# Performance work log

Measured on AMD Instinct MI355X. Metric: run time of the kernel, lower is better.

## Reference

```python
import jax, jax.numpy as jnp
import numpy as np

NUM_HEADS = 16
ROPE_BASE = 10000.0


def _rope_cos_sin(seq_len, head_dim, dtype):
    # Rotary (cramming-style): inv_freq over even indices, emb = cat(freqs, freqs)
    inv_freq = 1.0 / (ROPE_BASE ** (jnp.arange(0, head_dim, 2, dtype=jnp.float32) / head_dim))
    t = jnp.arange(seq_len, dtype=jnp.float32)
    freqs = jnp.einsum('i,j->ij', t, inv_freq)          # [S, d/2]
    emb = jnp.concatenate([freqs, freqs], axis=-1)      # [S, d]
    # broadcast over batch and heads: [1, S, 1, d]
    return jnp.cos(emb)[None, :, None, :].astype(dtype), jnp.sin(emb)[None, :, None, :].astype(dtype)


def _rotate_half(x):
    d = x.shape[-1] // 2
    return jnp.concatenate([-x[..., d:], x[..., :d]], axis=-1)


def setup_inputs() -> dict:
    key = jax.random.key(0)
    k1, k2, k3 = jax.random.split(key, 3)
    B, S, D = 4, 1024, 1024
    hidden_states = jax.random.normal(k1, (B, S, D), dtype=jnp.float32)
    Wqkv = jax.random.normal(k2, (3 * D, D), dtype=jnp.float32) * (D ** -0.5)
    bqkv = jax.random.normal(k3, (3 * D,), dtype=jnp.float32) * 0.02
    return {"hidden_states": hidden_states, "Wqkv": Wqkv, "bqkv": bqkv}


def reference(hidden_states, Wqkv, bqkv):
    B, S, D = hidden_states.shape
    H = NUM_HEADS
    hd = D // H

    # QKV projection (nn.Linear: x @ W.T + b)
    qkv = hidden_states @ Wqkv.T + bqkv                  # [B, S, 3D]
    qkv = qkv.reshape(B, S, 3, H, hd)
    q, k, v = qkv[:, :, 0], qkv[:, :, 1], qkv[:, :, 2]   # [B, S, H, hd]

    # Rotary embedding on q, k
    cos, sin = _rope_cos_sin(S, hd, q.dtype)
    q = q * cos + _rotate_half(q) * sin
    k = k * cos + _rotate_half(k) * sin

    # Causal scaled-dot-product attention (math of FlashAttention)
    scale = hd ** -0.5
    scores = jnp.einsum('bqhd,bkhd->bhqk', q, k) * scale  # [B, H, S, S]
    causal_mask = jnp.tril(jnp.ones((S, S), dtype=bool))
    scores = jnp.where(causal_mask, scores, jnp.finfo(scores.dtype).min)
    probs = jax.nn.softmax(scores, axis=-1)
    context = jnp.einsum('bhqk,bkhd->bqhd', probs, v)     # [B, S, H, hd]

    return context.reshape(B, S, D)
```

## Files before the change

kernel.cpp:

```cpp
#include <hip/hip_runtime.h>
#include <hip/hip_bf16.h>
#include <stdint.h>

typedef float f32x4 __attribute__((ext_vector_type(4)));
typedef __bf16 bf16x8 __attribute__((ext_vector_type(8)));

#define MFMA(a, b, c) __builtin_amdgcn_mfma_f32_16x16x32_bf16((a), (b), (c), 0, 0, 0)

__device__ __forceinline__ bf16x8 ld8(const void* p) { return *(const bf16x8*)p; }

__device__ __forceinline__ bf16x8 ld8f(const float* p) {
    float4 a = *(const float4*)p;
    float4 b = *(const float4*)(p + 4);
    bf16x8 r;
    r[0] = (__bf16)a.x; r[1] = (__bf16)a.y; r[2] = (__bf16)a.z; r[3] = (__bf16)a.w;
    r[4] = (__bf16)b.x; r[5] = (__bf16)b.y; r[6] = (__bf16)b.z; r[7] = (__bf16)b.w;
    return r;
}

__device__ __forceinline__ float fexp2(float x) {
    float r;
    asm("v_exp_f32 %0, %1" : "=v"(r) : "v"(x));
    return r;
}

__device__ __forceinline__ void gload16(const void* g, void* l) {
    __builtin_amdgcn_global_load_lds(
        (const __attribute__((address_space(1))) void*)g,
        (__attribute__((address_space(3))) void*)l, 16, 0, 0);
}

#define SW(row, cb) ((((row) * 128) + (cb)) ^ (((row) & 7) << 4))
#define SWV(row, cb) (((row) * 128) + ((cb) ^ (((((row) & 7) ^ (((row) >> 3) & 7))) << 4)))

#define SCALE2 0.18033688011112042f

__global__ void convert2_kernel(const float* __restrict__ X,
                                const float* __restrict__ W,
                                __bf16* __restrict__ out,
                                float2* __restrict__ rope) {
    const int bid = blockIdx.x;
    if (bid < 3584) {
        const size_t i = (size_t)(bid * 256 + threadIdx.x) * 8;
        const size_t NX = (size_t)4096 * 1024;
        if (i < NX) *(bf16x8*)(out + i) = ld8f(X + i);
        else        *(bf16x8*)(out + i) = ld8f(W + (i - NX));
    } else {
        const int idx = (bid - 3584) * 256 + threadIdx.x;
        const int t = idx >> 5, j = idx & 31;
        const float invf = __expf(-(float)j * 0.28782313662425575f);
        const float ang = (float)t * invf;
        float s, c;
        sincosf(ang, &s, &c);
        rope[idx] = make_float2(c, s);
    }
}

__global__ void rope_table_kernel(float2* __restrict__ rope) {
    const int idx = blockIdx.x * 256 + threadIdx.x;
    const int t = idx >> 5, j = idx & 31;
    const float invf = __expf(-(float)j * 0.28782313662425575f);
    const float ang = (float)t * invf;
    float s, c;
    sincosf(ang, &s, &c);
    rope[idx] = make_float2(c, s);
}

__global__ __launch_bounds__(256, 5) void qkv_rope_fast(
    const __bf16* __restrict__ Xb,
    const __bf16* __restrict__ Wb,
    const float* __restrict__ bias,
    const float2* __restrict__ rope,
    __bf16* __restrict__ QKV)
{
    __shared__ __align__(16) __bf16 Asm[128 * 64];
    __shared__ __align__(16) __bf16 Bsm[64 * 64];
    const int tid = threadIdx.x;
    const int w = tid >> 6, lane = tid & 63;
    const int fr = lane & 15, fq = lane >> 4;
    const int bn = blockIdx.x, bm = blockIdx.y;

    const int lrow = lane >> 3;
    const int scol = (((lane & 7) ^ lrow) & 7) * 8;
    const __bf16* ga = Xb + (size_t)(bm * 128 + w * 32 + lrow) * 1024 + scol;
    const __bf16* gb = Wb + (size_t)(bn * 64 + w * 16 + lrow) * 1024 + scol;
    __bf16* lA = &Asm[w * 2048];
    __bf16* lB = &Bsm[w * 1024];
    const uint8_t* Ab = (const uint8_t*)Asm;
    const uint8_t* Bb = (const uint8_t*)Bsm;

    const f32x4 fzero = {0.f, 0.f, 0.f, 0.f};
    f32x4 acc[2][4];
#pragma unroll
    for (int i = 0; i < 2; ++i)
#pragma unroll
        for (int j = 0; j < 4; ++j) acc[i][j] = fzero;

    for (int kt = 0; kt < 16; ++kt) {
        __syncthreads();
#pragma unroll
        for (int i = 0; i < 4; ++i)
            gload16(ga + (size_t)(i * 8) * 1024 + kt * 64, lA + i * 512);
#pragma unroll
        for (int i = 0; i < 2; ++i)
            gload16(gb + (size_t)(i * 8) * 1024 + kt * 64, lB + i * 512);
        __syncthreads();

#pragma unroll
        for (int kk = 0; kk < 2; ++kk) {
            bf16x8 af[2], bg[4];
#pragma unroll
            for (int mi = 0; mi < 2; ++mi)
                af[mi] = ld8(&Ab[SW(w * 32 + mi * 16 + fr, kk * 64 + fq * 16)]);
#pragma unroll
            for (int ni = 0; ni < 4; ++ni)
                bg[ni] = ld8(&Bb[SW(ni * 16 + fr, kk * 64 + fq * 16)]);
#pragma unroll
            for (int mi = 0; mi < 2; ++mi)
#pragma unroll
                for (int ni = 0; ni < 4; ++ni)
                    acc[mi][ni] = MFMA(af[mi], bg[ni], acc[mi][ni]);
        }
    }

    const int n0 = bn * 64;
    const int region = n0 >> 10;
    float bia[4];
#pragma unroll
    for (int ni = 0; ni < 4; ++ni) bia[ni] = bias[n0 + ni * 16 + fr];
#pragma unroll
    for (int mi = 0; mi < 2; ++mi) {
#pragma unroll
        for (int jr = 0; jr < 4; ++jr) {
            const int rg = bm * 128 + w * 32 + mi * 16 + fq * 4 + jr;
            const int spos = rg & 1023;
            float v0 = acc[mi][0][jr] + bia[0];
            float v1 = acc[mi][1][jr] + bia[1];
            float v2 = acc[mi][2][jr] + bia[2];
            float v3 = acc[mi][3][jr] + bia[3];
            if (region < 2) {
                const float2 cs0 = rope[spos * 32 + fr];
                const float2 cs1 = rope[spos * 32 + 16 + fr];
                const float t0 = v0, t1 = v1;
                v0 = t0 * cs0.x - v2 * cs0.y;
                v2 = v2 * cs0.x + t0 * cs0.y;
                v1 = t1 * cs1.x - v3 * cs1.y;
                v3 = v3 * cs1.x + t1 * cs1.y;
                if (region == 0) {
                    v0 *= SCALE2; v1 *= SCALE2; v2 *= SCALE2; v3 *= SCALE2;
                }
            }
            __bf16* op = QKV + (size_t)rg * 3072 + n0 + fr;
            op[0]  = (__bf16)v0;
            op[16] = (__bf16)v1;
            op[32] = (__bf16)v2;
            op[48] = (__bf16)v3;
        }
    }
}

__global__ __launch_bounds__(256, 2) void qkv_rope_slow(
    const float* __restrict__ X, const float* __restrict__ W,
    const float* __restrict__ bias, const float2* __restrict__ rope,
    __bf16* __restrict__ QKV)
{
    __shared__ __align__(16) __bf16 Asm[128 * 64];
    __shared__ __align__(16) __bf16 Bsm[128 * 64];
    const int tid = threadIdx.x;
    const int w = tid >> 6, lane = tid & 63;
    const int fr = lane & 15, fq = lane >> 4;
    const int wr = w >> 1, wn = w & 1;
    const int bn = blockIdx.x, bm = blockIdx.y;
    const int srow = w * 32 + (lane >> 3);
    const int scol = (lane & 7) * 8;
    const float* ga = X + (size_t)(bm * 128 + srow) * 1024 + scol;
    const float* gb = W + (size_t)(bn * 128 + srow) * 1024 + scol;
    const int ldst = w * 2048 + lane * 8;

    const f32x4 fzero = {0.f, 0.f, 0.f, 0.f};
    f32x4 acc[4][4];
#pragma unroll
    for (int i = 0; i < 4; ++i)
#pragma unroll
        for (int j = 0; j < 4; ++j) acc[i][j] = fzero;

    for (int kt = 0; kt < 16; ++kt) {
        bf16x8 av[4], bv[4];
#pragma unroll
        for (int i = 0; i < 4; ++i) {
            av[i] = ld8f(ga + (size_t)(i * 8) * 1024 + kt * 64);
            bv[i] = ld8f(gb + (size_t)(i * 8) * 1024 + kt * 64);
        }
        __syncthreads();
#pragma unroll
        for (int i = 0; i < 4; ++i) {
            *(bf16x8*)&Asm[ldst + i * 512] = av[i];
            *(bf16x8*)&Bsm[ldst + i * 512] = bv[i];
        }
        __syncthreads();
        bf16x8 af[4][2], bg[4][2];
#pragma unroll
        for (int mi = 0; mi < 4; ++mi)
#pragma unroll
            for (int kk = 0; kk < 2; ++kk)
                af[mi][kk] = ld8(&Asm[(wr * 64 + mi * 16 + fr) * 64 + kk * 32 + fq * 8]);
#pragma unroll
        for (int ni = 0; ni < 4; ++ni)
#pragma unroll
            for (int kk = 0; kk < 2; ++kk)
                bg[ni][kk] = ld8(&Bsm[(wn * 64 + ni * 16 + fr) * 64 + kk * 32 + fq * 8]);
#pragma unroll
        for (int kk = 0; kk < 2; ++kk)
#pragma unroll
            for (int mi = 0; mi < 4; ++mi)
#pragma unroll
                for (int ni = 0; ni < 4; ++ni)
                    acc[mi][ni] = MFMA(af[mi][kk], bg[ni][kk], acc[mi][ni]);
    }

    const int n0 = bn * 128 + wn * 64;
    const int region = n0 >> 10;
    float bia[4];
#pragma unroll
    for (int ni = 0; ni < 4; ++ni) bia[ni] = bias[n0 + ni * 16 + fr];
#pragma unroll
    for (int mi = 0; mi < 4; ++mi) {
#pragma unroll
        for (int jr = 0; jr < 4; ++jr) {
            const int rg = bm * 128 + wr * 64 + mi * 16 + fq * 4 + jr;
            const int spos = rg & 1023;
            float v0 = acc[mi][0][jr] + bia[0];
            float v1 = acc[mi][1][jr] + bia[1];
            float v2 = acc[mi][2][jr] + bia[2];
            float v3 = acc[mi][3][jr] + bia[3];
            if (region < 2) {
                const float2 cs0 = rope[spos * 32 + fr];
                const float2 cs1 = rope[spos * 32 + 16 + fr];
                const float t0 = v0, t1 = v1;
                v0 = t0 * cs0.x - v2 * cs0.y;
                v2 = v2 * cs0.x + t0 * cs0.y;
                v1 = t1 * cs1.x - v3 * cs1.y;
                v3 = v3 * cs1.x + t1 * cs1.y;
                if (region == 0) {
                    v0 *= SCALE2; v1 *= SCALE2; v2 *= SCALE2; v3 *= SCALE2;
                }
            }
            __bf16* op = QKV + (size_t)rg * 3072 + n0 + fr;
            op[0]  = (__bf16)v0;
            op[16] = (__bf16)v1;
            op[32] = (__bf16)v2;
            op[48] = (__bf16)v3;
        }
    }
}

__global__ __launch_bounds__(256, 2) void attn_kernel(
    const __bf16* __restrict__ QKV,
    float* __restrict__ Out)
{
    __shared__ __align__(16) uint8_t smem[49152];
    const int tid = threadIdx.x;
    const int w = tid >> 6, lane = tid & 63;
    const int fr = lane & 15, fq = lane >> 4;
    const int b = blockIdx.x >> 4, h = blockIdx.x & 15;
    const int jp = blockIdx.y;
    const int qtA = jp, qtB = 15 - jp;
    const int q0A = qtA * 64, q0B = qtB * 64;
    const __bf16* base = QKV + (size_t)b * 1024 * 3072 + h * 64;

    bf16x8 qfA[2], qfB[2];
#pragma unroll
    for (int kk = 0; kk < 2; ++kk) {
        qfA[kk] = ld8(base + (size_t)(q0A + w * 16 + fr) * 3072 + kk * 32 + fq * 8);
        qfB[kk] = ld8(base + (size_t)(q0B + w * 16 + fr) * 3072 + kk * 32 + fq * 8);
    }

    const f32x4 fzero = {0.f, 0.f, 0.f, 0.f};
    f32x4 oA[4], oB[4];
    float lA[4], lB[4];
#pragma unroll
    for (int jr = 0; jr < 4; ++jr) { lA[jr] = 0.f; lB[jr] = 0.f; }
#pragma unroll
    for (int fn = 0; fn < 4; ++fn) { oA[fn] = fzero; oB[fn] = fzero; }

    const int skey = tid >> 3;
    const int scol = (tid & 7) * 8;
    const int nkt = qtB + 1;
    const int pbA = 32768 + w * 4096;
    const int pbB = pbA + 2048;

    {
        const size_t g0 = (size_t)skey * 3072;
        const size_t g1 = (size_t)(32 + skey) * 3072;
        bf16x8 kxa = ld8(base + g0 + 1024 + scol);
        bf16x8 kxb = ld8(base + g1 + 1024 + scol);
        bf16x8 vxa = ld8(base + g0 + 2048 + scol);
        bf16x8 vxb = ld8(base + g1 + 2048 + scol);
        *(bf16x8*)&smem[SW(skey, scol * 2)] = kxa;
        *(bf16x8*)&smem[SW(32 + skey, scol * 2)] = kxb;
#pragma unroll
        for (int jj = 0; jj < 8; ++jj) {
            *(__bf16*)&smem[8192 + SWV(scol + jj, skey * 2)] = vxa[jj];
            *(__bf16*)&smem[8192 + SWV(scol + jj, (32 + skey) * 2)] = vxb[jj];
        }
    }
    __syncthreads();

#define MASKEXP_WRITE(SV, Q0, PB)                                              \
    do {                                                                       \
        if ((k0 + 63) > ((Q0) + w * 16)) {                                     \
            _Pragma("unroll") for (int ni = 0; ni < 4; ++ni)                   \
                _Pragma("unroll") for (int jr = 0; jr < 4; ++jr) {             \
                    const int rg = (Q0) + w * 16 + fq * 4 + jr;                \
                    const int kg = k0 + ni * 16 + fr;                          \
                    if (kg > rg) SV[ni][jr] = -1.0e30f;                        \
                }                                                              \
        }                                                                      \
        _Pragma("unroll") for (int jr = 0; jr < 4; ++jr) {                     \
            float ts = 0.f;                                                    \
            _Pragma("unroll") for (int ni = 0; ni < 4; ++ni) {                 \
                const float p = fexp2(SV[ni][jr]);                             \
                SV[ni][jr] = p;                                                \
                ts += p;                                                       \
            }                                                                  \
            (PB == pbA ? lA : lB)[jr] += ts;                                   \
        }                                                                      \
        _Pragma("unroll") for (int ni = 0; ni < 4; ++ni)                       \
            _Pragma("unroll") for (int jr = 0; jr < 4; ++jr)                   \
                *(__bf16*)&smem[(PB) + SW(fq * 4 + jr, (ni * 16 + fr) * 2)] =  \
                    (__bf16)SV[ni][jr];                                        \
    } while (0)

    for (int kt = 0; kt < nkt; ++kt) {
        const int k0 = kt * 64;
        const int cb = (kt & 1) << 14;
        const int nb = cb ^ 16384;
        const bool dual = (kt <= qtA);

        bf16x8 kxa, kxb, vxa, vxb;
        const bool pre = (kt + 1 < nkt);
        if (pre) {
            const size_t g0 = (size_t)(k0 + 64 + skey) * 3072;
            const size_t g1 = (size_t)(k0 + 96 + skey) * 3072;
            kxa = ld8(base + g0 + 1024 + scol);
            kxb = ld8(base + g1 + 1024 + scol);
            vxa = ld8(base + g0 + 2048 + scol);
            vxb = ld8(base + g1 + 2048 + scol);
        }

        f32x4 svA[4], svB[4];
#pragma unroll
        for (int ni = 0; ni < 4; ++ni) { svA[ni] = fzero; svB[ni] = fzero; }
#pragma unroll
        for (int kk = 0; kk < 2; ++kk) {
            bf16x8 kf[4];
#pragma unroll
            for (int ni = 0; ni < 4; ++ni)
                kf[ni] = ld8(&smem[cb + SW(ni * 16 + fr, (kk * 32 + fq * 8) * 2)]);
#pragma unroll
            for (int ni = 0; ni < 4; ++ni)
                svB[ni] = MFMA(qfB[kk], kf[ni], svB[ni]);
            if (dual) {
#pragma unroll
                for (int ni = 0; ni < 4; ++ni)
                    svA[ni] = MFMA(qfA[kk], kf[ni], svA[ni]);
            }
        }

        MASKEXP_WRITE(svB, q0B, pbB);
        if (dual) MASKEXP_WRITE(svA, q0A, pbA);

#pragma unroll
        for (int ks = 0; ks < 2; ++ks) {
            bf16x8 vf[4];
#pragma unroll
            for (int fn = 0; fn < 4; ++fn)
                vf[fn] = ld8(&smem[cb + 8192 + SWV(fn * 16 + fr, (ks * 32 + fq * 8) * 2)]);
            bf16x8 pfB = ld8(&smem[pbB + SW(fr, (ks * 32 + fq * 8) * 2)]);
#pragma unroll
            for (int fn = 0; fn < 4; ++fn)
                oB[fn] = MFMA(pfB, vf[fn], oB[fn]);
            if (dual) {
                bf16x8 pfA = ld8(&smem[pbA + SW(fr, (ks * 32 + fq * 8) * 2)]);
#pragma unroll
                for (int fn = 0; fn < 4; ++fn)
                    oA[fn] = MFMA(pfA, vf[fn], oA[fn]);
            }
        }

        if (pre) {
            *(bf16x8*)&smem[nb + SW(skey, scol * 2)] = kxa;
            *(bf16x8*)&smem[nb + SW(32 + skey, scol * 2)] = kxb;
#pragma unroll
            for (int jj = 0; jj < 8; ++jj) {
                *(__bf16*)&smem[nb + 8192 + SWV(scol + jj, skey * 2)] = vxa[jj];
                *(__bf16*)&smem[nb + 8192 + SWV(scol + jj, (32 + skey) * 2)] = vxb[jj];
            }
        }
        __syncthreads();
    }
#undef MASKEXP_WRITE

#pragma unroll
    for (int jr = 0; jr < 4; ++jr) {
        float la = lA[jr], lb = lB[jr];
#pragma unroll
        for (int off = 1; off < 16; off <<= 1) {
            la += __shfl_xor(la, off, 64);
            lb += __shfl_xor(lb, off, 64);
        }
        const float invA = 1.0f / fmaxf(la, 1.0e-20f);
        const float invB = 1.0f / fmaxf(lb, 1.0e-20f);
        const int rgA = q0A + w * 16 + fq * 4 + jr;
        const int rgB = q0B + w * 16 + fq * 4 + jr;
        float* opA = Out + (size_t)(b * 1024 + rgA) * 1024 + h * 64 + fr;
        float* opB = Out + (size_t)(b * 1024 + rgB) * 1024 + h * 64 + fr;
#pragma unroll
        for (int fn = 0; fn < 4; ++fn) {
            opA[fn * 16] = oA[fn][jr] * invA;
            opB[fn * 16] = oB[fn][jr] * invB;
        }
    }
}

extern "C" void kernel_launch(void* const* d_in, const int* in_sizes, int n_in,
                              void* d_out, int out_size, void* d_ws, size_t ws_size,
                              hipStream_t stream) {
    const float* X = (const float*)d_in[0];
    const float* W = (const float*)d_in[1];
    const float* bias = (const float*)d_in[2];
    float* out = (float*)d_out;

    const size_t ROPE = 262144;
    const size_t XB = ROPE + (size_t)4096 * 1024 * 2;
    const size_t WB = XB + (size_t)3072 * 1024 * 2;
    const size_t need_fast = WB + (size_t)3072 * 1024 * 2 + (size_t)4096 * 3072 * 2;

    float2* rope = (float2*)d_ws;

    if (ws_size >= need_fast) {
        __bf16* Xb = (__bf16*)((char*)d_ws + ROPE);
        __bf16* Wb = (__bf16*)((char*)d_ws + XB);
        __bf16* qkv = (__bf16*)((char*)d_ws + WB + (size_t)3072 * 1024 * 2);
        convert2_kernel<<<3712, 256, 0, stream>>>(X, W, Xb, rope);
        qkv_rope_fast<<<dim3(48, 32), 256, 0, stream>>>(Xb, Wb, bias, rope, qkv);
        attn_kernel<<<dim3(64, 8), 256, 0, stream>>>(qkv, out);
    } else {
        __bf16* qkv = (__bf16*)((char*)d_ws + ROPE);
        rope_table_kernel<<<128, 256, 0, stream>>>(rope);
        qkv_rope_slow<<<dim3(24, 32), 256, 0, stream>>>(X, W, bias, rope, qkv);
        attn_kernel<<<dim3(64, 8), 256, 0, stream>>>(qkv, out);
    }
}
```

Baseline: 77.53 us.

## Double-buffer LDS tiles in QKV projection GEMM to overlap loads with MFMA

Turns the A/B shared-memory tiles of the QKV+RoPE GEMM into two-stage buffers. The next K-tile's global-to-LDS loads are issued before the MFMAs on the current tile, and one barrier per iteration replaces two. The aim is to hide global load latency behind compute. The cost is doubled LDS per block, and the launch-bounds occupancy hint drops from 5 to 3 blocks per CU.

```diff
diff --git a/kernel.cpp b/kernel.cpp
--- a/kernel.cpp
+++ b/kernel.cpp
@@ -66,15 +66,15 @@
     rope[idx] = make_float2(c, s);
 }
 
-__global__ __launch_bounds__(256, 5) void qkv_rope_fast(
+__global__ __launch_bounds__(256, 3) void qkv_rope_fast(
     const __bf16* __restrict__ Xb,
     const __bf16* __restrict__ Wb,
     const float* __restrict__ bias,
     const float2* __restrict__ rope,
     __bf16* __restrict__ QKV)
 {
-    __shared__ __align__(16) __bf16 Asm[128 * 64];
-    __shared__ __align__(16) __bf16 Bsm[64 * 64];
+    __shared__ __align__(16) __bf16 Asm[2][128 * 64];
+    __shared__ __align__(16) __bf16 Bsm[2][64 * 64];
     const int tid = threadIdx.x;
     const int w = tid >> 6, lane = tid & 63;
     const int fr = lane & 15, fq = lane >> 4;
@@ -84,10 +84,16 @@
     const int scol = (((lane & 7) ^ lrow) & 7) * 8;
     const __bf16* ga = Xb + (size_t)(bm * 128 + w * 32 + lrow) * 1024 + scol;
     const __bf16* gb = Wb + (size_t)(bn * 64 + w * 16 + lrow) * 1024 + scol;
-    __bf16* lA = &Asm[w * 2048];
-    __bf16* lB = &Bsm[w * 1024];
-    const uint8_t* Ab = (const uint8_t*)Asm;
-    const uint8_t* Bb = (const uint8_t*)Bsm;
+
+#define STAGE(bb, kt)                                                          \
+    do {                                                                       \
+        _Pragma("unroll") for (int i = 0; i < 4; ++i)                          \
+            gload16(ga + (size_t)(i * 8) * 1024 + (kt) * 64,                   \
+                    &Asm[bb][w * 2048 + i * 512]);                             \
+        _Pragma("unroll") for (int i = 0; i < 2; ++i)                          \
+            gload16(gb + (size_t)(i * 8) * 1024 + (kt) * 64,                   \
+                    &Bsm[bb][w * 1024 + i * 512]);                             \
+    } while (0)
 
     const f32x4 fzero = {0.f, 0.f, 0.f, 0.f};
     f32x4 acc[2][4];
@@ -96,16 +102,15 @@
 #pragma unroll
         for (int j = 0; j < 4; ++j) acc[i][j] = fzero;
 
+    STAGE(0, 0);
+    __syncthreads();
+
+    int cur = 0;
     for (int kt = 0; kt < 16; ++kt) {
-        __syncthreads();
-#pragma unroll
-        for (int i = 0; i < 4; ++i)
-            gload16(ga + (size_t)(i * 8) * 1024 + kt * 64, lA + i * 512);
-#pragma unroll
-        for (int i = 0; i < 2; ++i)
-            gload16(gb + (size_t)(i * 8) * 1024 + kt * 64, lB + i * 512);
-        __syncthreads();
-
+        if (kt + 1 < 16) STAGE(cur ^ 1, kt + 1);
+
+        const uint8_t* Ab = (const uint8_t*)Asm[cur];
+        const uint8_t* Bb = (const uint8_t*)Bsm[cur];
 #pragma unroll
         for (int kk = 0; kk < 2; ++kk) {
             bf16x8 af[2], bg[4];
@@ -121,7 +126,11 @@
                 for (int ni = 0; ni < 4; ++ni)
                     acc[mi][ni] = MFMA(af[mi], bg[ni], acc[mi][ni]);
         }
-    }
+
+        __syncthreads();
+        cur ^= 1;
+    }
+#undef STAGE
 
     const int n0 = bn * 64;
     const int region = n0 >> 10;
```

Result: slower. 79.42 us (+2.4%).

## Enlarge QKV GEMM tile to 128x128 with two waves of 64x128 each

Applied to the files above, without the earlier changes.

The QKV projection kernel moves from 256-thread blocks computing 128x64 tiles to 128-thread blocks computing 128x128 tiles. Each wave now holds a 64x128 accumulator, which gives more MFMA work per LDS fragment load and halves the grid. The rope epilogue is restructured to handle two 64-column halves. This raises register pressure and lowers occupancy, and the grid shrinks to 768 blocks, which may underfill the GPU.

```diff
diff --git a/kernel.cpp b/kernel.cpp
--- a/kernel.cpp
+++ b/kernel.cpp
@@ -66,7 +66,7 @@
     rope[idx] = make_float2(c, s);
 }
 
-__global__ __launch_bounds__(256, 5) void qkv_rope_fast(
+__global__ __launch_bounds__(128, 2) void qkv_rope_fast(
     const __bf16* __restrict__ Xb,
     const __bf16* __restrict__ Wb,
     const float* __restrict__ bias,
@@ -74,87 +74,91 @@
     __bf16* __restrict__ QKV)
 {
     __shared__ __align__(16) __bf16 Asm[128 * 64];
-    __shared__ __align__(16) __bf16 Bsm[64 * 64];
+    __shared__ __align__(16) __bf16 Bsm[128 * 64];
     const int tid = threadIdx.x;
     const int w = tid >> 6, lane = tid & 63;
     const int fr = lane & 15, fq = lane >> 4;
     const int bn = blockIdx.x, bm = blockIdx.y;
 
-    const int lrow = lane >> 3;
-    const int scol = (((lane & 7) ^ lrow) & 7) * 8;
-    const __bf16* ga = Xb + (size_t)(bm * 128 + w * 32 + lrow) * 1024 + scol;
-    const __bf16* gb = Wb + (size_t)(bn * 64 + w * 16 + lrow) * 1024 + scol;
-    __bf16* lA = &Asm[w * 2048];
-    __bf16* lB = &Bsm[w * 1024];
+    const int trow = tid >> 3;
+    const int scol = (((tid & 7) ^ (trow & 7)) & 7) * 8;
+    const __bf16* ga = Xb + (size_t)(bm * 128 + trow) * 1024 + scol;
+    const __bf16* gb = Wb + (size_t)(bn * 128 + trow) * 1024 + scol;
+    const int lbase = w * 8 * 64;
     const uint8_t* Ab = (const uint8_t*)Asm;
     const uint8_t* Bb = (const uint8_t*)Bsm;
 
     const f32x4 fzero = {0.f, 0.f, 0.f, 0.f};
-    f32x4 acc[2][4];
-#pragma unroll
-    for (int i = 0; i < 2; ++i)
-#pragma unroll
-        for (int j = 0; j < 4; ++j) acc[i][j] = fzero;
+    f32x4 acc[4][8];
+#pragma unroll
+    for (int i = 0; i < 4; ++i)
+#pragma unroll
+        for (int j = 0; j < 8; ++j) acc[i][j] = fzero;
 
     for (int kt = 0; kt < 16; ++kt) {
         __syncthreads();
 #pragma unroll
-        for (int i = 0; i < 4; ++i)
-            gload16(ga + (size_t)(i * 8) * 1024 + kt * 64, lA + i * 512);
-#pragma unroll
-        for (int i = 0; i < 2; ++i)
-            gload16(gb + (size_t)(i * 8) * 1024 + kt * 64, lB + i * 512);
+        for (int i = 0; i < 8; ++i) {
+            gload16(ga + (size_t)(i * 16) * 1024 + kt * 64, &Asm[i * 1024 + lbase]);
+            gload16(gb + (size_t)(i * 16) * 1024 + kt * 64, &Bsm[i * 1024 + lbase]);
+        }
         __syncthreads();
 
 #pragma unroll
         for (int kk = 0; kk < 2; ++kk) {
-            bf16x8 af[2], bg[4];
-#pragma unroll
-            for (int mi = 0; mi < 2; ++mi)
-                af[mi] = ld8(&Ab[SW(w * 32 + mi * 16 + fr, kk * 64 + fq * 16)]);
-#pragma unroll
-            for (int ni = 0; ni < 4; ++ni)
+            bf16x8 af[4], bg[8];
+#pragma unroll
+            for (int mi = 0; mi < 4; ++mi)
+                af[mi] = ld8(&Ab[SW(w * 64 + mi * 16 + fr, kk * 64 + fq * 16)]);
+#pragma unroll
+            for (int ni = 0; ni < 8; ++ni)
                 bg[ni] = ld8(&Bb[SW(ni * 16 + fr, kk * 64 + fq * 16)]);
 #pragma unroll
-            for (int mi = 0; mi < 2; ++mi)
-#pragma unroll
-                for (int ni = 0; ni < 4; ++ni)
+            for (int mi = 0; mi < 4; ++mi)
+#pragma unroll
+                for (int ni = 0; ni < 8; ++ni)
                     acc[mi][ni] = MFMA(af[mi], bg[ni], acc[mi][ni]);
         }
     }
 
-    const int n0 = bn * 64;
-    const int region = n0 >> 10;
-    float bia[4];
-#pragma unroll
-    for (int ni = 0; ni < 4; ++ni) bia[ni] = bias[n0 + ni * 16 + fr];
-#pragma unroll
-    for (int mi = 0; mi < 2; ++mi) {
+    const int nbase = bn * 128;
+    const int region = nbase >> 10;
+    float bia[8];
+#pragma unroll
+    for (int ni = 0; ni < 8; ++ni) bia[ni] = bias[nbase + ni * 16 + fr];
+#pragma unroll
+    for (int mi = 0; mi < 4; ++mi) {
 #pragma unroll
         for (int jr = 0; jr < 4; ++jr) {
-            const int rg = bm * 128 + w * 32 + mi * 16 + fq * 4 + jr;
+            const int rg = bm * 128 + w * 64 + mi * 16 + fq * 4 + jr;
             const int spos = rg & 1023;
-            float v0 = acc[mi][0][jr] + bia[0];
-            float v1 = acc[mi][1][jr] + bia[1];
-            float v2 = acc[mi][2][jr] + bia[2];
-            float v3 = acc[mi][3][jr] + bia[3];
+            float2 cs0 = make_float2(1.f, 0.f), cs1 = make_float2(1.f, 0.f);
             if (region < 2) {
-                const float2 cs0 = rope[spos * 32 + fr];
-                const float2 cs1 = rope[spos * 32 + 16 + fr];
-                const float t0 = v0, t1 = v1;
-                v0 = t0 * cs0.x - v2 * cs0.y;
-                v2 = v2 * cs0.x + t0 * cs0.y;
-                v1 = t1 * cs1.x - v3 * cs1.y;
-                v3 = v3 * cs1.x + t1 * cs1.y;
-                if (region == 0) {
-                    v0 *= SCALE2; v1 *= SCALE2; v2 *= SCALE2; v3 *= SCALE2;
+                cs0 = rope[spos * 32 + fr];
+                cs1 = rope[spos * 32 + 16 + fr];
+            }
+#pragma unroll
+            for (int h = 0; h < 2; ++h) {
+                float v0 = acc[mi][h * 4 + 0][jr] + bia[h * 4 + 0];
+                float v1 = acc[mi][h * 4 + 1][jr] + bia[h * 4 + 1];
+                float v2 = acc[mi][h * 4 + 2][jr] + bia[h * 4 + 2];
+                float v3 = acc[mi][h * 4 + 3][jr] + bia[h * 4 + 3];
+                if (region < 2) {
+                    const float t0 = v0, t1 = v1;
+                    v0 = t0 * cs0.x - v2 * cs0.y;
+                    v2 = v2 * cs0.x + t0 * cs0.y;
+                    v1 = t1 * cs1.x - v3 * cs1.y;
+                    v3 = v3 * cs1.x + t1 * cs1.y;
+                    if (region == 0) {
+                        v0 *= SCALE2; v1 *= SCALE2; v2 *= SCALE2; v3 *= SCALE2;
+                    }
                 }
-            }
-            __bf16* op = QKV + (size_t)rg * 3072 + n0 + fr;
-            op[0]  = (__bf16)v0;
-            op[16] = (__bf16)v1;
-            op[32] = (__bf16)v2;
-            op[48] = (__bf16)v3;
+                __bf16* op = QKV + (size_t)rg * 3072 + nbase + h * 64 + fr;
+                op[0]  = (__bf16)v0;
+                op[16] = (__bf16)v1;
+                op[32] = (__bf16)v2;
+                op[48] = (__bf16)v3;
+            }
         }
     }
 }
@@ -443,7 +447,7 @@
         __bf16* Wb = (__bf16*)((char*)d_ws + XB);
         __bf16* qkv = (__bf16*)((char*)d_ws + WB + (size_t)3072 * 1024 * 2);
         convert2_kernel<<<3712, 256, 0, stream>>>(X, W, Xb, rope);
-        qkv_rope_fast<<<dim3(48, 32), 256, 0, stream>>>(Xb, Wb, bias, rope, qkv);
+        qkv_rope_fast<<<dim3(24, 32), 128, 0, stream>>>(Xb, Wb, bias, rope, qkv);
         attn_kernel<<<dim3(64, 8), 256, 0, stream>>>(qkv, out);
     } else {
         __bf16* qkv = (__bf16*)((char*)d_ws + ROPE);
```

New measurement: 72.82 us. -6.1%, faster.
